# Optimization experiments

Measured on AMD Instinct MI355X. Metric: run time of the kernel, lower is better.

The kernel has to match this reference:

```python
import jax, jax.numpy as jnp
import numpy as np

D_MODEL = 1024
NUM_HEADS = 16
D_INT = D_MODEL // NUM_HEADS  # 64
B, T = 2, 2048


def justnorm(x):
    return x / jnp.linalg.norm(x, axis=-1, keepdims=True)


def rope_tables(seq_len, dim, base=10000.0):
    inv_freq = 1.0 / (base ** (jnp.arange(0, dim, 2, dtype=jnp.float32) / dim))
    freqs = jnp.arange(seq_len, dtype=jnp.float32)[:, None] * inv_freq[None, :]  # [T, dim/2]
    emb = jnp.concatenate([freqs, freqs], axis=-1)  # [T, dim]
    return jnp.cos(emb), jnp.sin(emb)


def rotate_half(x):
    h = x.shape[-1] // 2
    return jnp.concatenate([-x[..., h:], x[..., :h]], axis=-1)


def setup_inputs() -> dict:
    key = jax.random.key(0)
    ks = jax.random.split(key, 8)
    s = D_MODEL ** -0.5
    return {
        "x": jax.random.normal(ks[0], (B, T, D_MODEL), jnp.float32),
        "Wqkv": jax.random.normal(ks[1], (NUM_HEADS, 3 * D_INT, D_MODEL), jnp.float32) * s,
        "sqk": (D_MODEL ** -0.5) * jnp.ones((NUM_HEADS, D_INT), jnp.float32),
        "W_O": jax.random.normal(ks[2], (D_MODEL, D_MODEL), jnp.float32) * s,
        "attn_alpha": (D_MODEL ** -0.5) * jnp.ones((D_MODEL,), jnp.float32),
        "Wu_w": jax.random.normal(ks[3], (8 * D_MODEL, D_MODEL), jnp.float32) * s,
        "Wu_b": jnp.zeros((8 * D_MODEL,), jnp.float32),
        "suv": jnp.ones((8 * D_MODEL,), jnp.float32),
        "Wv_w": jax.random.normal(ks[4], (D_MODEL, 4 * D_MODEL), jnp.float32) * (4 * D_MODEL) ** -0.5,
        "Wv_b": jnp.zeros((D_MODEL,), jnp.float32),
        "mlp_alpha": jnp.ones((D_MODEL,), jnp.float32),
    }


def reference(x, Wqkv, sqk, W_O, attn_alpha, Wu_w, Wu_b, suv, Wv_w, Wv_b, mlp_alpha):
    Bq, Tq, C = x.shape

    # --- attention (all heads batched) ---
    qkv = jnp.einsum('btc,hec->bhte', x, Wqkv)  # [B,H,T,3*d_i]
    Q, K, V = jnp.split(qkv, 3, axis=-1)        # each [B,H,T,d_i]

    cos, sin = rope_tables(Tq, D_INT)           # [T,d_i]
    Q = Q * cos + rotate_half(Q) * sin
    K = K * cos + rotate_half(K) * sin

    sqk_b = sqk[None, :, None, :]
    Q = justnorm(Q) * sqk_b
    K = justnorm(K) * sqk_b

    scale = C ** 0.5  # as written in the source (scale=C**0.5)
    scores = jnp.einsum('bhqd,bhkd->bhqk', Q, K) * scale
    causal = jnp.tril(jnp.ones((Tq, Tq), dtype=bool))
    scores = jnp.where(causal, scores, jnp.finfo(scores.dtype).min)
    attn = jax.nn.softmax(scores, axis=-1)
    out = jnp.einsum('bhqk,bhkd->bhqd', attn, V)       # [B,H,T,d_i]
    t = out.transpose(0, 2, 1, 3).reshape(Bq, Tq, C)   # concat heads

    t = justnorm(t) @ W_O.T

    # alpha-residual mix (attn): init_value=0.05, init_scaling=d_model**-0.5
    lr = jnp.abs(attn_alpha * (0.05 / (C ** -0.5)))
    A = justnorm(x)
    Bn = justnorm(t)
    x2 = justnorm(A + lr * (Bn - A))

    # --- SwiGLU-style FFN ---
    uv = x2 @ Wu_w.T + Wu_b                     # [B,T,8*d_model]
    suv_s = suv * (1.0 * (C ** 0.5))            # suv_init_value/scaling = 1
    uv = suv_s * uv
    tn = justnorm(uv)
    u, v = jnp.split(tn, 2, axis=-1)
    res = u * jax.nn.silu(v)
    t2 = res @ Wv_w.T + Wv_b

    lr2 = jnp.abs(mlp_alpha * 0.05)             # mlp init_value=0.05, scaling=1
    A2 = justnorm(x2)
    B2 = justnorm(t2)
    return justnorm(A2 + lr2 * (B2 - A2))
```

## Files before the change

### kernel.cpp

```cpp
#include <hip/hip_runtime.h>
#include <cstdint>
#include <cstddef>

#define DEVI __device__ __forceinline__

typedef __attribute__((ext_vector_type(8))) short s16x8;
typedef __attribute__((ext_vector_type(8))) unsigned short u16x8;
typedef __attribute__((ext_vector_type(4))) float f32x4;
typedef unsigned short u16;

static constexpr int Bc = 2, Tc = 2048, Hc = 16, DMc = 1024;
static constexpr int VTS = 2064;

DEVI float bf2f(u16 u){ unsigned int x = ((unsigned int)u) << 16; return __builtin_bit_cast(float, x); }
DEVI u16 f2bf(float f){
  unsigned int u = __builtin_bit_cast(unsigned int, f);
  u += 0x7FFFu + ((u >> 16) & 1u);
  return (u16)(u >> 16);
}

DEVI float waveSum(float v){
  #pragma unroll
  for (int m = 1; m < 64; m <<= 1) v += __shfl_xor(v, m);
  return v;
}

DEVI void gload16(const void* g, void* l){
  __builtin_amdgcn_global_load_lds((const __attribute__((address_space(1))) void*)g,
                                   (__attribute__((address_space(3))) void*)l, 16, 0, 0);
}

__global__ __launch_bounds__(256) void cvt_f32_bf16(const float* __restrict__ in,
                                                    u16* __restrict__ out, int n4){
  int i = blockIdx.x * blockDim.x + threadIdx.x;
  int stride = gridDim.x * blockDim.x;
  for (int idx = i; idx < n4; idx += stride){
    float4 v = ((const float4*)in)[idx];
    ushort4 o;
    o.x = f2bf(v.x); o.y = f2bf(v.y); o.z = f2bf(v.z); o.w = f2bf(v.w);
    ((ushort4*)out)[idx] = o;
  }
}

template<int EPI>
__global__ __launch_bounds__(256) void gemm_bt(
    const u16* __restrict__ A, int lda, const u16* __restrict__ W,
    float* __restrict__ outF, u16* __restrict__ outB, u16* __restrict__ outB2,
    const float* __restrict__ bias, const float* __restrict__ scale, float smul,
    int M, int N, int K)
{
  __shared__ u16 lA[128 * 64];
  __shared__ u16 lB[128 * 64];
  const int tid = threadIdx.x, lane = tid & 63;
  const int wave = tid >> 6, wm = wave >> 1, wn = wave & 1;
  const int g = lane >> 4, cl = lane & 15;
  const int F = blockIdx.y * gridDim.x + blockIdx.x;
  const int xcd = F & 7, i0 = F >> 3;
  const int NCH = gridDim.x >> 3;
  const int n0 = (xcd * NCH + i0 % NCH) * 128;
  const int m0 = (i0 / NCH) * 128;
  f32x4 acc[4][4] = {};
  const int kT = K >> 6;
  char* lAc = (char*)lA;
  char* lBc = (char*)lB;
  const int wuni = (tid & ~63);

  for (int kt = 0; kt < kT; ++kt){
    const int k0 = kt << 6;
    __syncthreads();
    #pragma unroll
    for (int j = 0; j < 4; ++j){
      const int idx = j * 256 + tid;
      const int row = idx >> 3;
      const int sb = ((idx & 7) ^ (row & 7)) << 3;
      gload16(A + (size_t)(m0 + row) * lda + k0 + sb,
              lAc + ((j * 256 + wuni) << 4));
    }
    #pragma unroll
    for (int j = 0; j < 4; ++j){
      const int idx = j * 256 + tid;
      const int row = idx >> 3;
      const int sb = ((idx & 7) ^ (row & 7)) << 3;
      gload16(W + (size_t)(n0 + row) * K + k0 + sb,
              lBc + ((j * 256 + wuni) << 4));
    }
    __syncthreads();

    #pragma unroll
    for (int kk = 0; kk < 2; ++kk){
      s16x8 aF[4], bF[4];
      #pragma unroll
      for (int i = 0; i < 4; ++i){
        const int ra = wm * 64 + i * 16 + cl;
        aF[i] = *(const s16x8*)&lA[ra * 64 + (((kk * 4 + g) ^ (ra & 7)) << 3)];
      }
      #pragma unroll
      for (int j = 0; j < 4; ++j){
        const int rbr = wn * 64 + j * 16 + cl;
        bF[j] = *(const s16x8*)&lB[rbr * 64 + (((kk * 4 + g) ^ (rbr & 7)) << 3)];
      }
      #pragma unroll
      for (int i = 0; i < 4; ++i)
        #pragma unroll
        for (int j = 0; j < 4; ++j)
          acc[i][j] = __builtin_amdgcn_mfma_f32_16x16x32_bf16(aF[i], bF[j], acc[i][j], 0, 0, 0);
    }
  }

  const int rb = m0 + wm * 64 + (g << 2);
  const int cb = n0 + wn * 64 + cl;
  #pragma unroll
  for (int i = 0; i < 4; ++i){
    #pragma unroll
    for (int j = 0; j < 4; ++j){
      #pragma unroll
      for (int r = 0; r < 4; ++r){
        const int row = rb + i * 16 + r;
        const int col = cb + j * 16;
        float v = acc[i][j][r];
        if (EPI == 0){
          if (bias) v += bias[col];
          outF[(size_t)row * N + col] = v;
        } else if (EPI == 1){
          const int b = row >> 11;
          const int t = row & (Tc - 1);
          const int h = col / 192;
          const int e = col - h * 192;
          const int bh = b * Hc + h;
          if (e < 128){
            outB[((size_t)bh * Tc + t) * 128 + e] = f2bf(v);
          } else {
            outB2[((size_t)bh * 64 + (e - 128)) * VTS + t] = f2bf(v);
          }
        } else {
          v = (v + bias[col]) * (scale[col] * smul);
          outB[(size_t)row * N + col] = f2bf(v);
        }
      }
    }
  }
}

__global__ __launch_bounds__(256) void gemm64_bt(
    const u16* __restrict__ A, int lda, const u16* __restrict__ W, int ldw,
    float* __restrict__ outF, const float* __restrict__ bias,
    int M, int N, int K)
{
  __shared__ u16 lA[64 * 64];
  __shared__ u16 lB[64 * 64];
  const int tid = threadIdx.x, lane = tid & 63;
  const int wave = tid >> 6, wm = wave >> 1, wn = wave & 1;
  const int g = lane >> 4, cl = lane & 15;
  const int nwg = gridDim.x * gridDim.y;
  int flat = blockIdx.y * gridDim.x + blockIdx.x;
  flat = (flat & 7) * (nwg >> 3) + (flat >> 3);
  const int n0 = (flat % gridDim.x) * 64;
  const int m0 = (flat / gridDim.x) * 64;
  f32x4 acc[2][2] = {};
  const int kT = K >> 6;
  const int wuni = tid & ~63;

  for (int kt = 0; kt < kT; ++kt){
    const int k0 = kt << 6;
    __syncthreads();
    #pragma unroll
    for (int it = 0; it < 2; ++it){
      const int idx = it * 256 + tid;
      const int row = idx >> 3;
      const int sb = ((idx & 7) ^ (row & 7)) << 3;
      gload16(A + (size_t)(m0 + row) * lda + k0 + sb,
              (char*)lA + ((it * 256 + wuni) << 4));
      gload16(W + (size_t)(n0 + row) * ldw + k0 + sb,
              (char*)lB + ((it * 256 + wuni) << 4));
    }
    __syncthreads();

    #pragma unroll
    for (int kk = 0; kk < 2; ++kk){
      s16x8 aF[2], bF[2];
      #pragma unroll
      for (int i = 0; i < 2; ++i){
        const int ra = wm * 32 + i * 16 + cl;
        aF[i] = *(const s16x8*)&lA[ra * 64 + (((kk * 4 + g) ^ (ra & 7)) << 3)];
        const int rbr = wn * 32 + i * 16 + cl;
        bF[i] = *(const s16x8*)&lB[rbr * 64 + (((kk * 4 + g) ^ (rbr & 7)) << 3)];
      }
      #pragma unroll
      for (int i = 0; i < 2; ++i)
        #pragma unroll
        for (int j = 0; j < 2; ++j)
          acc[i][j] = __builtin_amdgcn_mfma_f32_16x16x32_bf16(aF[i], bF[j], acc[i][j], 0, 0, 0);
    }
  }

  const int rb = m0 + wm * 32 + (g << 2);
  const int cb = n0 + wn * 32 + cl;
  #pragma unroll
  for (int i = 0; i < 2; ++i){
    #pragma unroll
    for (int j = 0; j < 2; ++j){
      #pragma unroll
      for (int r = 0; r < 4; ++r){
        const int row = rb + i * 16 + r;
        const int col = cb + j * 16;
        float v = acc[i][j][r];
        if (bias) v += bias[col];
        outF[(size_t)row * N + col] = v;
      }
    }
  }
}

__global__ __launch_bounds__(256) void rope_norm(u16* __restrict__ qk,
                                                 const float* __restrict__ sqk){
  const int lane = threadIdx.x & 63;
  const int idx = blockIdx.x * 4 + (threadIdx.x >> 6);
  const int t = idx & (Tc - 1);
  const int h = (idx >> 11) & (Hc - 1);
  u16* row = qk + (size_t)idx * 128;
  float q = bf2f(row[lane]), k = bf2f(row[64 + lane]);
  const int fi = lane & 31;
  float invf = powf(10000.0f, -(float)fi / 32.0f);
  float ang = (float)t * invf;
  float sn, cs;
  sincosf(ang, &sn, &cs);
  float qo = __shfl_xor(q, 32), ko = __shfl_xor(k, 32);
  float rq = (lane < 32) ? -qo : qo;
  float rk = (lane < 32) ? -ko : ko;
  float qn = q * cs + rq * sn;
  float kn = k * cs + rk * sn;
  float sq = waveSum(qn * qn), sk = waveSum(kn * kn);
  float scl = sqk[h * 64 + lane];
  row[lane]      = f2bf(qn / sqrtf(sq) * scl);
  row[64 + lane] = f2bf(kn / sqrtf(sk) * scl);
}

__global__ __launch_bounds__(256) void attn_kernel(const u16* __restrict__ qk,
                                                   const u16* __restrict__ vt,
                                                   float* __restrict__ o){
  __shared__ u16 Kt[2][4096];
  __shared__ u16 Vt[2][4096];
  __shared__ u16 Pt[4][1024];

  const int tid = threadIdx.x, lane = tid & 63, wave = tid >> 6;
  const int wuni = tid & ~63;
  const int bh = blockIdx.y;
  const int g = lane >> 4, cl = lane & 15;
  const u16* qkb = qk + (size_t)bh * Tc * 128;
  const u16* vtb = vt + (size_t)bh * 64 * VTS;
  const int b = bh / Hc, h = bh % Hc;

  auto stage = [&](int sel, int kb){
    #pragma unroll
    for (int it = 0; it < 2; ++it){
      const int idx = it * 256 + tid;
      const int row = idx >> 3, blk = idx & 7;
      const int sb = (blk ^ (row & 7)) << 3;
      gload16(qkb + (size_t)(kb + row) * 128 + 64 + sb,
              (char*)Kt[sel] + ((it * 256 + wuni) << 4));
      gload16(vtb + (size_t)row * VTS + kb + sb,
              (char*)Vt[sel] + ((it * 256 + wuni) << 4));
    }
  };

  #pragma unroll 1
  for (int half = 0; half < 2; ++half){
    const int cq = (half == 0) ? (int)blockIdx.x : 31 - (int)blockIdx.x;
    const int q0b = cq * 64;
    const int qw = q0b + wave * 16;
    const int nsteps = cq + 1;

    s16x8 qF[2];
    {
      const u16* qrow = qkb + (size_t)(qw + cl) * 128 + (g << 3);
      qF[0] = *(const s16x8*)qrow;
      qF[1] = *(const s16x8*)(qrow + 32);
    }
    f32x4 oF[4] = {};
    float mrow[4], lrow[4];
    #pragma unroll
    for (int r = 0; r < 4; ++r){ mrow[r] = -3.0e38f; lrow[r] = 0.0f; }

    auto compute = [&](int sel, int kb){
      const u16* Kl = Kt[sel];
      const u16* Vl = Vt[sel];
      u16* pw = Pt[wave];
      f32x4 sF[4] = {};
      #pragma unroll
      for (int c16 = 0; c16 < 4; ++c16){
        const int kr = c16 * 16 + cl;
        s16x8 k0 = *(const s16x8*)&Kl[kr * 64 + (((g)     ^ (cl & 7)) << 3)];
        s16x8 k1 = *(const s16x8*)&Kl[kr * 64 + (((4 + g) ^ (cl & 7)) << 3)];
        sF[c16] = __builtin_amdgcn_mfma_f32_16x16x32_bf16(qF[0], k0, sF[c16], 0, 0, 0);
        sF[c16] = __builtin_amdgcn_mfma_f32_16x16x32_bf16(qF[1], k1, sF[c16], 0, 0, 0);
      }
      #pragma unroll
      for (int r = 0; r < 4; ++r){
        const int qg = qw + g * 4 + r;
        float s0 = sF[0][r] * 32.0f; if (kb + cl      > qg) s0 = -3.0e38f;
        float s1 = sF[1][r] * 32.0f; if (kb + 16 + cl > qg) s1 = -3.0e38f;
        float s2 = sF[2][r] * 32.0f; if (kb + 32 + cl > qg) s2 = -3.0e38f;
        float s3 = sF[3][r] * 32.0f; if (kb + 48 + cl > qg) s3 = -3.0e38f;
        float mx = fmaxf(fmaxf(s0, s1), fmaxf(s2, s3));
        mx = fmaxf(mx, __shfl_xor(mx, 1));
        mx = fmaxf(mx, __shfl_xor(mx, 2));
        mx = fmaxf(mx, __shfl_xor(mx, 4));
        mx = fmaxf(mx, __shfl_xor(mx, 8));
        const float mnew = fmaxf(mrow[r], mx);
        const float al = __expf(mrow[r] - mnew);
        const float p0 = __expf(s0 - mnew);
        const float p1 = __expf(s1 - mnew);
        const float p2 = __expf(s2 - mnew);
        const float p3 = __expf(s3 - mnew);
        float ps = (p0 + p1) + (p2 + p3);
        ps += __shfl_xor(ps, 1);
        ps += __shfl_xor(ps, 2);
        ps += __shfl_xor(ps, 4);
        ps += __shfl_xor(ps, 8);
        lrow[r] = lrow[r] * al + ps;
        mrow[r] = mnew;
        oF[0][r] *= al; oF[1][r] *= al; oF[2][r] *= al; oF[3][r] *= al;
        const int rp = g * 4 + r;
        const int rsw = (rp & 7);
        pw[rp * 64 + ((((cl >> 3)    ) ^ rsw) << 3) + (cl & 7)] = f2bf(p0);
        pw[rp * 64 + ((((cl >> 3) + 2) ^ rsw) << 3) + (cl & 7)] = f2bf(p1);
        pw[rp * 64 + ((((cl >> 3) + 4) ^ rsw) << 3) + (cl & 7)] = f2bf(p2);
        pw[rp * 64 + ((((cl >> 3) + 6) ^ rsw) << 3) + (cl & 7)] = f2bf(p3);
      }
      #pragma unroll
      for (int ksub = 0; ksub < 2; ++ksub){
        s16x8 pF = *(const s16x8*)&pw[cl * 64 + (((ksub * 4 + g) ^ (cl & 7)) << 3)];
        #pragma unroll
        for (int d0 = 0; d0 < 4; ++d0){
          s16x8 vF = *(const s16x8*)&Vl[(d0 * 16 + cl) * 64 + (((ksub * 4 + g) ^ (cl & 7)) << 3)];
          oF[d0] = __builtin_amdgcn_mfma_f32_16x16x32_bf16(pF, vF, oF[d0], 0, 0, 0);
        }
      }
    };

    stage(0, 0);
    __syncthreads();
    for (int kt = 0; kt < nsteps; ++kt){
      const int sel = kt & 1;
      const int kb = kt * 64;
      if (kt + 1 < nsteps) stage(sel ^ 1, (kt + 1) * 64);
      compute(sel, kb);
      __syncthreads();
    }

    float invl[4];
    #pragma unroll
    for (int r = 0; r < 4; ++r) invl[r] = 1.0f / lrow[r];
    #pragma unroll
    for (int d0 = 0; d0 < 4; ++d0){
      #pragma unroll
      for (int r = 0; r < 4; ++r){
        const int qg = qw + g * 4 + r;
        o[((size_t)(b * Tc + qg)) * DMc + h * 64 + d0 * 16 + cl] = oF[d0][r] * invl[r];
      }
    }
  }
}

__global__ __launch_bounds__(256) void rownorm1024(const float* __restrict__ in,
                                                   u16* __restrict__ out){
  const int row = blockIdx.x, tid = threadIdx.x;
  const float* r = in + (size_t)row * 1024;
  float v[4]; float ss = 0.0f;
  #pragma unroll
  for (int i = 0; i < 4; ++i){ v[i] = r[tid + i * 256]; ss += v[i] * v[i]; }
  __shared__ float red[4];
  ss = waveSum(ss);
  if ((tid & 63) == 0) red[tid >> 6] = ss;
  __syncthreads();
  const float tot = red[0] + red[1] + red[2] + red[3];
  const float inv = 1.0f / sqrtf(tot);
  #pragma unroll
  for (int i = 0; i < 4; ++i) out[(size_t)row * 1024 + tid + i * 256] = f2bf(v[i] * inv);
}

__global__ __launch_bounds__(256) void x2_kernel(const float* __restrict__ x,
                                                 const float* __restrict__ t,
                                                 const float* __restrict__ alpha,
                                                 float* __restrict__ x2f,
                                                 u16* __restrict__ x2b){
  const int row = blockIdx.x, tid = threadIdx.x, lane = tid & 63, wv = tid >> 6;
  const float* xr = x + (size_t)row * 1024;
  const float* tr = t + (size_t)row * 1024;
  float xv[4], tv[4]; float sx = 0.0f, st = 0.0f;
  #pragma unroll
  for (int i = 0; i < 4; ++i){
    xv[i] = xr[tid + i * 256]; sx += xv[i] * xv[i];
    tv[i] = tr[tid + i * 256]; st += tv[i] * tv[i];
  }
  __shared__ float red[8];
  sx = waveSum(sx); st = waveSum(st);
  if (lane == 0){ red[wv] = sx; red[4 + wv] = st; }
  __syncthreads();
  sx = red[0] + red[1] + red[2] + red[3];
  st = red[4] + red[5] + red[6] + red[7];
  const float ix = 1.0f / sqrtf(sx), it = 1.0f / sqrtf(st);
  float yv[4]; float sy = 0.0f;
  #pragma unroll
  for (int i = 0; i < 4; ++i){
    const int c = tid + i * 256;
    const float lr = fabsf(alpha[c] * 1.6f);
    const float a = xv[i] * ix, bn = tv[i] * it;
    yv[i] = a + lr * (bn - a);
    sy += yv[i] * yv[i];
  }
  sy = waveSum(sy);
  __syncthreads();
  if (lane == 0) red[wv] = sy;
  __syncthreads();
  sy = red[0] + red[1] + red[2] + red[3];
  const float iy = 1.0f / sqrtf(sy);
  #pragma unroll
  for (int i = 0; i < 4; ++i){
    const int c = tid + i * 256;
    const float v = yv[i] * iy;
    x2f[(size_t)row * 1024 + c] = v;
    x2b[(size_t)row * 1024 + c] = f2bf(v);
  }
}

__global__ __launch_bounds__(256) void uvres_kernel(u16* __restrict__ uv){
  const int row = blockIdx.x, tid = threadIdx.x;
  u16* p = uv + (size_t)row * 8192;
  float uvv[32]; float ss = 0.0f;
  const u16x8* su = (const u16x8*)(p + tid * 16);
  const u16x8* sv = (const u16x8*)(p + 4096 + tid * 16);
  u16x8 a0 = su[0], a1 = su[1], b0 = sv[0], b1 = sv[1];
  #pragma unroll
  for (int j = 0; j < 8; ++j){
    uvv[j]      = bf2f(a0[j]); uvv[8 + j]  = bf2f(a1[j]);
    uvv[16 + j] = bf2f(b0[j]); uvv[24 + j] = bf2f(b1[j]);
  }
  #pragma unroll
  for (int j = 0; j < 32; ++j) ss += uvv[j] * uvv[j];
  __shared__ float red[4];
  ss = waveSum(ss);
  if ((tid & 63) == 0) red[tid >> 6] = ss;
  __syncthreads();
  const float tot = red[0] + red[1] + red[2] + red[3];
  const float inv = 1.0f / sqrtf(tot);
  #pragma unroll
  for (int j = 0; j < 16; ++j){
    const float un = uvv[j] * inv;
    const float vn = uvv[16 + j] * inv;
    const float sil = vn / (1.0f + expf(-vn));
    p[tid * 16 + j] = f2bf(un * sil);
  }
}

__global__ __launch_bounds__(256) void final_kernel(const float* __restrict__ x2,
                                                    const float* __restrict__ t2,
                                                    const float* __restrict__ alpha,
                                                    float* __restrict__ out){
  const int row = blockIdx.x, tid = threadIdx.x, lane = tid & 63, wv = tid >> 6;
  const float* a = x2 + (size_t)row * 1024;
  const float* b = t2 + (size_t)row * 1024;
  float av[4], bv[4]; float sa = 0.0f, sb = 0.0f;
  #pragma unroll
  for (int i = 0; i < 4; ++i){
    av[i] = a[tid + i * 256]; sa += av[i] * av[i];
    bv[i] = b[tid + i * 256]; sb += bv[i] * bv[i];
  }
  __shared__ float red[8];
  sa = waveSum(sa); sb = waveSum(sb);
  if (lane == 0){ red[wv] = sa; red[4 + wv] = sb; }
  __syncthreads();
  sa = red[0] + red[1] + red[2] + red[3];
  sb = red[4] + red[5] + red[6] + red[7];
  const float ia = 1.0f / sqrtf(sa), ib = 1.0f / sqrtf(sb);
  float yv[4]; float sy = 0.0f;
  #pragma unroll
  for (int i = 0; i < 4; ++i){
    const int c = tid + i * 256;
    const float lr = fabsf(alpha[c] * 0.05f);
    const float an = av[i] * ia, bn = bv[i] * ib;
    yv[i] = an + lr * (bn - an);
    sy += yv[i] * yv[i];
  }
  sy = waveSum(sy);
  __syncthreads();
  if (lane == 0) red[wv] = sy;
  __syncthreads();
  sy = red[0] + red[1] + red[2] + red[3];
  const float iy = 1.0f / sqrtf(sy);
  #pragma unroll
  for (int i = 0; i < 4; ++i)
    out[(size_t)row * 1024 + tid + i * 256] = yv[i] * iy;
}

extern "C" void kernel_launch(void* const* d_in, const int* in_sizes, int n_in,
                              void* d_out, int out_size, void* d_ws, size_t ws_size,
                              hipStream_t stream) {
  const float* x          = (const float*)d_in[0];
  const float* Wqkv       = (const float*)d_in[1];
  const float* sqk        = (const float*)d_in[2];
  const float* W_O        = (const float*)d_in[3];
  const float* attn_alpha = (const float*)d_in[4];
  const float* Wu_w       = (const float*)d_in[5];
  const float* Wu_b       = (const float*)d_in[6];
  const float* suv        = (const float*)d_in[7];
  const float* Wv_w       = (const float*)d_in[8];
  const float* Wv_b       = (const float*)d_in[9];
  const float* mlp_alpha  = (const float*)d_in[10];
  float* out = (float*)d_out;

  char* ws = (char*)d_ws;
  u16*   wbuf = (u16*)(ws);
  u16*   abuf = (u16*)(ws + 16777216);
  u16*   qkb  = (u16*)(ws + 25165824);
  float* tbuf = (float*)(ws + 25165824);
  float* aout = (float*)(ws + 50331648);
  float* x2f  = (float*)(ws + 50331648);
  u16*   uvb  = (u16*)(ws + 67108864);
  u16*   vtb  = (u16*)(ws + 67108864);

  const int M = Bc * Tc;

  auto cvt = [&](const float* in, u16* o, int n){
    int n4 = n / 4;
    int blocks = (n4 + 255) / 256;
    if (blocks > 4096) blocks = 4096;
    cvt_f32_bf16<<<dim3(blocks), dim3(256), 0, stream>>>(in, o, n4);
  };

  cvt(x, abuf, M * DMc);
  cvt(Wqkv, wbuf, Hc * 192 * DMc);
  gemm_bt<1><<<dim3(3072 / 128, M / 128), 256, 0, stream>>>(
      abuf, DMc, wbuf, nullptr, qkb, vtb, nullptr, nullptr, 0.0f, M, 3072, DMc);

  rope_norm<<<dim3(Bc * Hc * Tc / 4), 256, 0, stream>>>(qkb, sqk);

  attn_kernel<<<dim3(Tc / 128, Bc * Hc), 256, 0, stream>>>(qkb, vtb, aout);

  rownorm1024<<<dim3(M), 256, 0, stream>>>(aout, abuf);
  cvt(W_O, wbuf, DMc * DMc);
  gemm64_bt<<<dim3(DMc / 64, M / 64), 256, 0, stream>>>(
      abuf, DMc, wbuf, DMc, tbuf, nullptr, M, DMc, DMc);

  x2_kernel<<<dim3(M), 256, 0, stream>>>(x, tbuf, attn_alpha, x2f, abuf);

  cvt(Wu_w, wbuf, 8192 * DMc);
  gemm_bt<2><<<dim3(8192 / 128, M / 128), 256, 0, stream>>>(
      abuf, DMc, wbuf, nullptr, uvb, nullptr, Wu_b, suv, 32.0f, M, 8192, DMc);

  uvres_kernel<<<dim3(M), 256, 0, stream>>>(uvb);

  cvt(Wv_w, wbuf, DMc * 4096);
  gemm64_bt<<<dim3(DMc / 64, M / 64), 256, 0, stream>>>(
      uvb, 8192, wbuf, 4096, tbuf, Wv_b, M, DMc, 4096);

  final_kernel<<<dim3(M), 256, 0, stream>>>(x2f, tbuf, mlp_alpha, out);
}
```

Measured before the change: 365.1 us.

## Drop online-softmax max tracking and precompute RoPE cos/sin table

Attention now computes exp2 of the scaled scores directly, with no running row max or rescaling. The row-sum reduction across lanes happens once at the end instead of every key tile. This relies on Q and K being L2-normalised and scaled by sqk, which bounds the logits. It could overflow if sqk were much larger than in the test setup. Separately, a small kernel builds a cos/sin table in workspace, so rope_norm loads it instead of calling powf and sincosf in every row.

```diff
diff --git a/kernel.cpp b/kernel.cpp
--- a/kernel.cpp
+++ b/kernel.cpp
@@ -211,8 +211,18 @@
   }
 }
 
+__global__ __launch_bounds__(256) void rope_table(float2* __restrict__ tab){
+  const int i = blockIdx.x * 256 + threadIdx.x;
+  const int t = i >> 5, fi = i & 31;
+  const float invf = powf(10000.0f, -(float)fi / 32.0f);
+  float sn, cs;
+  sincosf((float)t * invf, &sn, &cs);
+  tab[i] = make_float2(cs, sn);
+}
+
 __global__ __launch_bounds__(256) void rope_norm(u16* __restrict__ qk,
-                                                 const float* __restrict__ sqk){
+                                                 const float* __restrict__ sqk,
+                                                 const float2* __restrict__ tab){
   const int lane = threadIdx.x & 63;
   const int idx = blockIdx.x * 4 + (threadIdx.x >> 6);
   const int t = idx & (Tc - 1);
@@ -220,10 +230,8 @@
   u16* row = qk + (size_t)idx * 128;
   float q = bf2f(row[lane]), k = bf2f(row[64 + lane]);
   const int fi = lane & 31;
-  float invf = powf(10000.0f, -(float)fi / 32.0f);
-  float ang = (float)t * invf;
-  float sn, cs;
-  sincosf(ang, &sn, &cs);
+  const float2 cssn = tab[t * 32 + fi];
+  const float cs = cssn.x, sn = cssn.y;
   float qo = __shfl_xor(q, 32), ko = __shfl_xor(k, 32);
   float rq = (lane < 32) ? -qo : qo;
   float rk = (lane < 32) ? -ko : ko;
@@ -277,9 +285,7 @@
       qF[1] = *(const s16x8*)(qrow + 32);
     }
     f32x4 oF[4] = {};
-    float mrow[4], lrow[4];
-    #pragma unroll
-    for (int r = 0; r < 4; ++r){ mrow[r] = -3.0e38f; lrow[r] = 0.0f; }
+    float lsum[4] = {0.0f, 0.0f, 0.0f, 0.0f};
 
     auto compute = [&](int sel, int kb){
       const u16* Kl = Kt[sel];
@@ -294,32 +300,15 @@
         sF[c16] = __builtin_amdgcn_mfma_f32_16x16x32_bf16(qF[0], k0, sF[c16], 0, 0, 0);
         sF[c16] = __builtin_amdgcn_mfma_f32_16x16x32_bf16(qF[1], k1, sF[c16], 0, 0, 0);
       }
+      const float c = 46.16624f;
       #pragma unroll
       for (int r = 0; r < 4; ++r){
         const int qg = qw + g * 4 + r;
-        float s0 = sF[0][r] * 32.0f; if (kb + cl      > qg) s0 = -3.0e38f;
-        float s1 = sF[1][r] * 32.0f; if (kb + 16 + cl > qg) s1 = -3.0e38f;
-        float s2 = sF[2][r] * 32.0f; if (kb + 32 + cl > qg) s2 = -3.0e38f;
-        float s3 = sF[3][r] * 32.0f; if (kb + 48 + cl > qg) s3 = -3.0e38f;
-        float mx = fmaxf(fmaxf(s0, s1), fmaxf(s2, s3));
-        mx = fmaxf(mx, __shfl_xor(mx, 1));
-        mx = fmaxf(mx, __shfl_xor(mx, 2));
-        mx = fmaxf(mx, __shfl_xor(mx, 4));
-        mx = fmaxf(mx, __shfl_xor(mx, 8));
-        const float mnew = fmaxf(mrow[r], mx);
-        const float al = __expf(mrow[r] - mnew);
-        const float p0 = __expf(s0 - mnew);
-        const float p1 = __expf(s1 - mnew);
-        const float p2 = __expf(s2 - mnew);
-        const float p3 = __expf(s3 - mnew);
-        float ps = (p0 + p1) + (p2 + p3);
-        ps += __shfl_xor(ps, 1);
-        ps += __shfl_xor(ps, 2);
-        ps += __shfl_xor(ps, 4);
-        ps += __shfl_xor(ps, 8);
-        lrow[r] = lrow[r] * al + ps;
-        mrow[r] = mnew;
-        oF[0][r] *= al; oF[1][r] *= al; oF[2][r] *= al; oF[3][r] *= al;
+        const float p0 = (kb + cl      > qg) ? 0.0f : exp2f(sF[0][r] * c);
+        const float p1 = (kb + 16 + cl > qg) ? 0.0f : exp2f(sF[1][r] * c);
+        const float p2 = (kb + 32 + cl > qg) ? 0.0f : exp2f(sF[2][r] * c);
+        const float p3 = (kb + 48 + cl > qg) ? 0.0f : exp2f(sF[3][r] * c);
+        lsum[r] += (p0 + p1) + (p2 + p3);
         const int rp = g * 4 + r;
         const int rsw = (rp & 7);
         pw[rp * 64 + ((((cl >> 3)    ) ^ rsw) << 3) + (cl & 7)] = f2bf(p0);
@@ -350,7 +339,14 @@
 
     float invl[4];
     #pragma unroll
-    for (int r = 0; r < 4; ++r) invl[r] = 1.0f / lrow[r];
+    for (int r = 0; r < 4; ++r){
+      float l = lsum[r];
+      l += __shfl_xor(l, 1);
+      l += __shfl_xor(l, 2);
+      l += __shfl_xor(l, 4);
+      l += __shfl_xor(l, 8);
+      invl[r] = 1.0f / l;
+    }
     #pragma unroll
     for (int d0 = 0; d0 < 4; ++d0){
       #pragma unroll
@@ -533,7 +529,8 @@
   gemm_bt<1><<<dim3(3072 / 128, M / 128), 256, 0, stream>>>(
       abuf, DMc, wbuf, nullptr, qkb, vtb, nullptr, nullptr, 0.0f, M, 3072, DMc);
 
-  rope_norm<<<dim3(Bc * Hc * Tc / 4), 256, 0, stream>>>(qkb, sqk);
+  rope_table<<<dim3(Tc * 32 / 256), 256, 0, stream>>>((float2*)wbuf);
+  rope_norm<<<dim3(Bc * Hc * Tc / 4), 256, 0, stream>>>(qkb, sqk, (const float2*)wbuf);
 
   attn_kernel<<<dim3(Tc / 128, Bc * Hc), 256, 0, stream>>>(qkb, vtb, aout);
 
```

After: 335.7 us. 1.09x faster.
